# Optimization experiments

Hardware: AMD Instinct MI355X
Metric: run time of the kernel (lower is better)

Reference implementation:

```python
import jax, jax.numpy as jnp
import numpy as np

D = 128
L_SIZE = 65536
C_SIZE = 32768
E = 262144
N_ITERS = 4


def _mlp(x, w1, b1, w2, b2):
    # 2-layer satbench MLP: Linear -> relu -> Linear
    return jax.nn.relu(x @ w1 + b1) @ w2 + b2


def setup_inputs() -> dict:
    key = jax.random.key(0)
    ks = iter(jax.random.split(key, 32))

    def lin(fi, fo):
        # torch nn.Linear default init, stored as (in, out)
        bound = 1.0 / np.sqrt(fi)
        w = jax.random.uniform(next(ks), (fi, fo), minval=-bound, maxval=bound, dtype=jnp.float32)
        b = jax.random.uniform(next(ks), (fo,), minval=-bound, maxval=bound, dtype=jnp.float32)
        return w, b

    s = np.sqrt(2.0 / D).astype(np.float32)
    inp = {}
    inp['l_edge_index'] = jax.random.randint(next(ks), (E,), 0, L_SIZE, dtype=jnp.int64)
    inp['c_edge_index'] = jax.random.randint(next(ks), (E,), 0, C_SIZE, dtype=jnp.int64)
    inp['l_init'] = jax.random.normal(next(ks), (1, D), dtype=jnp.float32) * s
    inp['c_init'] = jax.random.normal(next(ks), (1, D), dtype=jnp.float32) * s
    inp['w_l2c1'], inp['b_l2c1'] = lin(D, D)
    inp['w_l2c2'], inp['b_l2c2'] = lin(D, D)
    inp['w_c2l1'], inp['b_c2l1'] = lin(D, D)
    inp['w_c2l2'], inp['b_c2l2'] = lin(D, D)
    inp['w_l2l1'], inp['b_l2l1'] = lin(D, D)
    inp['w_l2l2'], inp['b_l2l2'] = lin(D, D)
    inp['w_cu'], inp['b_cu'] = lin(2 * D, D)
    inp['w_lu'], inp['b_lu'] = lin(3 * D, D)
    inp['l_size'] = L_SIZE
    inp['c_size'] = C_SIZE
    return inp


def reference(l_edge_index, c_edge_index, l_init, c_init,
              w_l2c1, b_l2c1, w_l2c2, b_l2c2,
              w_c2l1, b_c2l1, w_c2l2, b_c2l2,
              w_l2l1, b_l2l1, w_l2l2, b_l2l2,
              w_cu, b_cu, w_lu, b_lu, l_size, c_size):
    d = l_init.shape[1]
    ones = jnp.ones((l_edge_index.shape[0], 1), dtype=l_init.dtype)
    l_deg = jax.ops.segment_sum(ones, l_edge_index, num_segments=l_size)   # (L,1)
    c_deg = jax.ops.segment_sum(ones, c_edge_index, num_segments=c_size)   # (C,1)
    degree_norm = jnp.sqrt(l_deg[l_edge_index]) * jnp.sqrt(c_deg[c_edge_index])  # (E,1)

    l_emb = jnp.tile(l_init, (l_size, 1))  # (L,d)
    c_emb = jnp.tile(c_init, (c_size, 1))  # (C,d)

    def step(carry, _):
        l_emb, c_emb = carry
        l2c_msg = _mlp(l_emb, w_l2c1, b_l2c1, w_l2c2, b_l2c2)[l_edge_index]  # (E,d)
        c2l_msg = _mlp(c_emb, w_c2l1, b_c2l1, w_c2l2, b_c2l2)[c_edge_index]  # (E,d)
        # swap positive/negative literal partner embeddings (pairs are adjacent rows)
        l2l_in = l_emb.reshape(l_size // 2, 2, d)[:, ::-1, :].reshape(l_size, d)
        l2l_msg = _mlp(l2l_in, w_l2l1, b_l2l1, w_l2l2, b_l2l2)              # (L,d)
        l2c_aggr = jax.ops.segment_sum(l2c_msg / degree_norm, c_edge_index, num_segments=c_size)
        c_new = jnp.concatenate([c_emb, l2c_aggr], axis=1) @ w_cu + b_cu
        c2l_aggr = jax.ops.segment_sum(c2l_msg / degree_norm, l_edge_index, num_segments=l_size)
        l_new = jnp.concatenate([l_emb, c2l_aggr, l2l_msg], axis=1) @ w_lu + b_lu
        return (l_new, c_new), None

    (l_emb, c_emb), _ = jax.lax.scan(step, (l_emb, c_emb), None, length=N_ITERS)
    return l_emb
```

## Files before the change

kernel.cpp:

```cpp
#include <hip/hip_runtime.h>
#include <hip/hip_bf16.h>

#define D_ 128
#define L_ 65536
#define C_ 32768
#define E_ 262144

typedef __hip_bfloat16 bf16;
typedef __attribute__((ext_vector_type(8))) short short8;
typedef __attribute__((ext_vector_type(4))) float f32x4;

__global__ void detect_k(const unsigned short* __restrict__ wmem,
                         const int* __restrict__ li, int* __restrict__ flags) {
    int t = blockIdx.x * 512 + threadIdx.x;
    if (t < 8192) {
        unsigned short h = wmem[2 * t];
        float v = __bfloat162float(*(const bf16*)&h);
        if (!(fabsf(v) < 0.5f)) atomicOr(&flags[0], 1);
    }
    if (t < 2048) {
        if (li[2 * t + 1] != 0) atomicOr(&flags[1], 1);
    }
}

__device__ __forceinline__ void split2(float v, unsigned short& h, unsigned short& l) {
    bf16 bh = __float2bfloat16(v);
    float fh = __bfloat162float(bh);
    bf16 bl = __float2bfloat16(v - fh);
    h = *(unsigned short*)&bh;
    l = *(unsigned short*)&bl;
}

__device__ __forceinline__ float ldf(const void* s, int i, int isf32) {
    return isf32 ? ((const float*)s)[i] : __bfloat162float(((const bf16*)s)[i]);
}

__global__ void fixdeg_k(const int* __restrict__ ls, const int* __restrict__ cs,
                         int* __restrict__ ld_idx, int* __restrict__ cd_idx,
                         int* __restrict__ ldeg, int* __restrict__ cdeg,
                         const int* __restrict__ flags) {
    int i = blockIdx.x * 256 + threadIdx.x;
    int is32 = flags[1];
    if (i < E_) {
        int v = is32 ? ls[i] : ls[2 * i];
        v = min(max(v, 0), L_ - 1);
        ld_idx[i] = v;
        atomicAdd(&ldeg[v], 1);
    } else {
        int j = i - E_;
        int v = is32 ? cs[j] : cs[2 * j];
        v = min(max(v, 0), C_ - 1);
        cd_idx[j] = v;
        atomicAdd(&cdeg[v], 1);
    }
}

__global__ void cvtwb_k(const void* s0, const void* s1, const void* s2, const void* s3,
                        const void* s4, const void* s5, const void* s6, const void* s7,
                        const void* t0, const void* t1, const void* t2, const void* t3,
                        const void* t4, const void* t5, const void* t6, const void* t7,
                        unsigned short* __restrict__ hi, unsigned short* __restrict__ lo,
                        float* __restrict__ bb, const int* __restrict__ flags) {
    int i = blockIdx.x * 256 + threadIdx.x;
    int isf = flags[0];
    if (i >= 180224) {
        int j = i - 180224;
        const void* src;
        switch (j >> 7) {
            case 0: src = t0; break; case 1: src = t1; break;
            case 2: src = t2; break; case 3: src = t3; break;
            case 4: src = t4; break; case 5: src = t5; break;
            case 6: src = t6; break; default: src = t7; break;
        }
        bb[j] = ldf(src, j & 127, isf);
        return;
    }
    const void* src; int K, base;
    if      (i <  16384) { src = s0; K = 128; base = 0; }
    else if (i <  32768) { src = s1; K = 128; base = 16384; }
    else if (i <  49152) { src = s2; K = 128; base = 32768; }
    else if (i <  65536) { src = s3; K = 128; base = 49152; }
    else if (i <  81920) { src = s4; K = 128; base = 65536; }
    else if (i <  98304) { src = s5; K = 128; base = 81920; }
    else if (i < 131072) { src = s6; K = 256; base = 98304; }
    else                 { src = s7; K = 384; base = 131072; }
    int e = i - base;
    int k = e >> 7, n = e & 127;
    float v = ldf(src, e, isf);
    unsigned short h, l;
    split2(v, h, l);
    hi[base + n * K + k] = h;
    lo[base + n * K + k] = l;
}

__global__ void init2_k(const void* __restrict__ lv, const void* __restrict__ cv,
                        float* __restrict__ lemb, float* __restrict__ cemb,
                        const int* __restrict__ flags) {
    int i = blockIdx.x * 256 + threadIdx.x;
    int isf = flags[0];
    if (i < L_ * D_) lemb[i] = ldf(lv, i & (D_ - 1), isf);
    else             cemb[i - L_ * D_] = ldf(cv, i & (D_ - 1), isf);
}

__global__ void scan1b_k(const int* __restrict__ ldeg, const int* __restrict__ cdeg,
                         int* __restrict__ lout, int* __restrict__ cout,
                         int* __restrict__ bsumL, int* __restrict__ bsumC) {
    __shared__ int s[256];
    const int* in; int* out; int* bs; int tile;
    if (blockIdx.x < 256) { in = ldeg; out = lout; bs = bsumL; tile = blockIdx.x; }
    else                  { in = cdeg; out = cout; bs = bsumC; tile = blockIdx.x - 256; }
    int i = tile * 256 + threadIdx.x;
    int v = in[i];
    s[threadIdx.x] = v;
    __syncthreads();
#pragma unroll
    for (int off = 1; off < 256; off <<= 1) {
        int t = (threadIdx.x >= off) ? s[threadIdx.x - off] : 0;
        __syncthreads();
        s[threadIdx.x] += t;
        __syncthreads();
    }
    out[i] = s[threadIdx.x] - v;
    if (threadIdx.x == 255) bs[tile] = s[255];
}

__global__ void scan2b_k(int* __restrict__ bL, int* __restrict__ bC) {
    __shared__ int s[256];
    int* b = blockIdx.x ? bC : bL;
    int nb = blockIdx.x ? 128 : 256;
    int v = (threadIdx.x < nb) ? b[threadIdx.x] : 0;
    s[threadIdx.x] = v;
    __syncthreads();
#pragma unroll
    for (int off = 1; off < 256; off <<= 1) {
        int t = (threadIdx.x >= off) ? s[threadIdx.x - off] : 0;
        __syncthreads();
        s[threadIdx.x] += t;
        __syncthreads();
    }
    if (threadIdx.x < nb) b[threadIdx.x] = s[threadIdx.x] - v;
}

__global__ void scan3b_k(int* __restrict__ lptr, int* __restrict__ cptr,
                         const int* __restrict__ bsumL, const int* __restrict__ bsumC,
                         int* __restrict__ lcur, int* __restrict__ ccur,
                         const int* __restrict__ ldeg, const int* __restrict__ cdeg,
                         float* __restrict__ invsq_l, float* __restrict__ invsq_c) {
    int b = blockIdx.x, t = threadIdx.x;
    if (b < 256) {
        int i = b * 256 + t;
        int v = lptr[i] + bsumL[b];
        lptr[i] = v; lcur[i] = v;
        int d = ldeg[i];
        invsq_l[i] = d ? rsqrtf((float)d) : 0.0f;
    } else {
        int i = (b - 256) * 256 + t;
        int v = cptr[i] + bsumC[b - 256];
        cptr[i] = v; ccur[i] = v;
        int d = cdeg[i];
        invsq_c[i] = d ? rsqrtf((float)d) : 0.0f;
    }
}

__global__ void place_k(const int* __restrict__ li, const int* __restrict__ ci,
                        int* __restrict__ lcur, int* __restrict__ ccur,
                        int* __restrict__ l_other, int* __restrict__ c_other) {
    int e = blockIdx.x * 256 + threadIdx.x;
    if (e >= E_) return;
    int l = li[e], c = ci[e];
    int p = atomicAdd(&ccur[c], 1);
    c_other[p] = l;
    int q = atomicAdd(&lcur[l], 1);
    l_other[q] = c;
}

__global__ __launch_bounds__(256) void gather2_k(
    const int* __restrict__ cptr, const int* __restrict__ cdeg, const int* __restrict__ c_other,
    const float* __restrict__ lmsg, const float* __restrict__ invsq_c, float* __restrict__ caggr,
    const int* __restrict__ lptr, const int* __restrict__ ldeg, const int* __restrict__ l_other,
    const float* __restrict__ cmsg, const float* __restrict__ invsq_l, float* __restrict__ laggr,
    int nC) {
    int node = (blockIdx.x * 256 + threadIdx.x) >> 6;
    int lane = threadIdx.x & 63;
    bool cside = node < nC;
    int j = cside ? node : node - nC;
    const int* ptr = cside ? cptr : lptr;
    const int* dg  = cside ? cdeg : ldeg;
    const int* oth = cside ? c_other : l_other;
    const float* msg = cside ? lmsg : cmsg;
    float sc = (cside ? invsq_c : invsq_l)[j];
    float* out = cside ? caggr : laggr;
    int s = ptr[j], cnt = dg[j];
    float2 a0 = {0.f, 0.f}, a1 = {0.f, 0.f};
    int k = 0;
    for (; k + 2 <= cnt; k += 2) {
        int o0 = oth[s + k], o1 = oth[s + k + 1];
        const float2 m0 = *(const float2*)&msg[(size_t)o0 * D_ + 2 * lane];
        const float2 m1 = *(const float2*)&msg[(size_t)o1 * D_ + 2 * lane];
        a0.x += m0.x; a0.y += m0.y;
        a1.x += m1.x; a1.y += m1.y;
    }
    if (k < cnt) {
        int o = oth[s + k];
        const float2 m = *(const float2*)&msg[(size_t)o * D_ + 2 * lane];
        a0.x += m.x; a0.y += m.y;
    }
    a0.x = (a0.x + a1.x) * sc;
    a0.y = (a0.y + a1.y) * sc;
    *(float2*)&out[(size_t)j * D_ + 2 * lane] = a0;
}

__global__ __launch_bounds__(256, 2) void mlp3_k(
    const float* __restrict__ l_cur, const float* __restrict__ c_cur,
    const unsigned short* __restrict__ wt_hi, const unsigned short* __restrict__ wt_lo,
    const float* __restrict__ bb,
    const float* __restrict__ invsq_l, const float* __restrict__ invsq_c,
    float* __restrict__ l_msg, float* __restrict__ c_msg, float* __restrict__ l2lb,
    int nL, int nC) {
    __shared__ char smem[66048];
    unsigned short (*a_hi)[40] = (unsigned short(*)[40])(smem);
    unsigned short (*a_lo)[40] = (unsigned short(*)[40])(smem + 10240);
    unsigned short (*b_hi)[40] = (unsigned short(*)[40])(smem + 20480);
    unsigned short (*b_lo)[40] = (unsigned short(*)[40])(smem + 30720);
    unsigned short* h_hi = (unsigned short*)(smem);
    unsigned short* h_lo = (unsigned short*)(smem + 32768);
    float* scv = (float*)(smem + 65536);

    int b = blockIdx.x, seg, tile;
    if (b < nL)           { seg = 0; tile = b; }
    else if (b < nL + nC) { seg = 1; tile = b - nL; }
    else                  { seg = 2; tile = b - nL - nC; }
    const float* A = (seg == 1) ? c_cur : l_cur;
    float* outp = (seg == 0) ? l_msg : (seg == 1) ? c_msg : l2lb;
    const float* invsq = (seg == 0) ? invsq_l : (seg == 1) ? invsq_c : nullptr;
    const unsigned short* W1h = wt_hi + seg * 32768;
    const unsigned short* W1l = wt_lo + seg * 32768;
    const unsigned short* W2h = W1h + 16384;
    const unsigned short* W2l = W1l + 16384;
    const float* b1v = bb + seg * 256;
    const float* b2v = b1v + 128;
    const int swap = (seg == 2);

    const int t = threadIdx.x;
    const int br0 = tile * 128;
    const int w = t >> 6, lane = t & 63;
    const int wr = w >> 1, wc = w & 1;
    const int quad = lane >> 4, cl = lane & 15;

    if (t < 128) scv[t] = invsq ? invsq[br0 + t] : 1.0f;

    f32x4 acc[4][4];
#pragma unroll
    for (int i = 0; i < 4; i++)
#pragma unroll
        for (int j = 0; j < 4; j++) acc[i][j] = (f32x4){0.f, 0.f, 0.f, 0.f};

    for (int kt = 0; kt < 128; kt += 32) {
#pragma unroll
        for (int i = 0; i < 4; i++) {
            int f = t + 256 * i;
            int r = f >> 3, kq = f & 7;
            int gr = br0 + r;
            if (swap) gr ^= 1;
            const float4 v = *(const float4*)&A[(size_t)gr * D_ + kt + 4 * kq];
            unsigned short h0, l0, h1, l1, h2, l2, h3, l3;
            split2(v.x, h0, l0); split2(v.y, h1, l1);
            split2(v.z, h2, l2); split2(v.w, h3, l3);
            *(ushort4*)&a_hi[r][4 * kq] = make_ushort4(h0, h1, h2, h3);
            *(ushort4*)&a_lo[r][4 * kq] = make_ushort4(l0, l1, l2, l3);
            *(ushort4*)&b_hi[r][4 * kq] = *(const ushort4*)&W1h[(size_t)r * 128 + kt + 4 * kq];
            *(ushort4*)&b_lo[r][4 * kq] = *(const ushort4*)&W1l[(size_t)r * 128 + kt + 4 * kq];
        }
        __syncthreads();
        short8 af_h[4], af_l[4];
#pragma unroll
        for (int i = 0; i < 4; i++) {
            int row = 64 * wr + 16 * i + cl;
            af_h[i] = *(const short8*)&a_hi[row][quad * 8];
            af_l[i] = *(const short8*)&a_lo[row][quad * 8];
        }
#pragma unroll
        for (int j = 0; j < 4; j++) {
            int col = 64 * wc + 16 * j + cl;
            short8 bf_h = *(const short8*)&b_hi[col][quad * 8];
            short8 bf_l = *(const short8*)&b_lo[col][quad * 8];
#pragma unroll
            for (int i = 0; i < 4; i++) {
                acc[i][j] = __builtin_amdgcn_mfma_f32_16x16x32_bf16(af_h[i], bf_h, acc[i][j], 0, 0, 0);
                acc[i][j] = __builtin_amdgcn_mfma_f32_16x16x32_bf16(af_h[i], bf_l, acc[i][j], 0, 0, 0);
                acc[i][j] = __builtin_amdgcn_mfma_f32_16x16x32_bf16(af_l[i], bf_h, acc[i][j], 0, 0, 0);
            }
        }
        __syncthreads();
    }
#pragma unroll
    for (int j = 0; j < 4; j++) {
        int col = 64 * wc + 16 * j + cl;
        float bv = b1v[col];
        int g = col >> 3, go = col & 7;
#pragma unroll
        for (int i = 0; i < 4; i++) {
            int rloc = 64 * wr + 16 * i + quad * 4;
#pragma unroll
            for (int rg = 0; rg < 4; rg++) {
                float v = fmaxf(acc[i][j][rg] + bv, 0.0f);
                unsigned short hh, ll;
                split2(v, hh, ll);
                int r = rloc + rg;
                int off = r * 128 + ((g ^ (r & 15)) << 3) + go;
                h_hi[off] = hh;
                h_lo[off] = ll;
            }
        }
    }
    __syncthreads();
#pragma unroll
    for (int i = 0; i < 4; i++)
#pragma unroll
        for (int j = 0; j < 4; j++) acc[i][j] = (f32x4){0.f, 0.f, 0.f, 0.f};

    for (int kt = 0; kt < 128; kt += 32) {
        short8 af_h[4], af_l[4];
        int gbase = (kt >> 3) + quad;
#pragma unroll
        for (int i = 0; i < 4; i++) {
            int r = 64 * wr + 16 * i + cl;
            int off = r * 128 + ((gbase ^ cl) << 3);
            af_h[i] = *(const short8*)&h_hi[off];
            af_l[i] = *(const short8*)&h_lo[off];
        }
#pragma unroll
        for (int j = 0; j < 4; j++) {
            int col = 64 * wc + 16 * j + cl;
            const short8 bf_h = *(const short8*)&W2h[(size_t)col * 128 + kt + quad * 8];
            const short8 bf_l = *(const short8*)&W2l[(size_t)col * 128 + kt + quad * 8];
#pragma unroll
            for (int i = 0; i < 4; i++) {
                acc[i][j] = __builtin_amdgcn_mfma_f32_16x16x32_bf16(af_h[i], bf_h, acc[i][j], 0, 0, 0);
                acc[i][j] = __builtin_amdgcn_mfma_f32_16x16x32_bf16(af_h[i], bf_l, acc[i][j], 0, 0, 0);
                acc[i][j] = __builtin_amdgcn_mfma_f32_16x16x32_bf16(af_l[i], bf_h, acc[i][j], 0, 0, 0);
            }
        }
    }
#pragma unroll
    for (int j = 0; j < 4; j++) {
        int col = 64 * wc + 16 * j + cl;
        float bv = b2v[col];
#pragma unroll
        for (int i = 0; i < 4; i++) {
            int rloc = 64 * wr + 16 * i + quad * 4;
#pragma unroll
            for (int rg = 0; rg < 4; rg++)
                outp[(size_t)(br0 + rloc + rg) * D_ + col] = (acc[i][j][rg] + bv) * scv[rloc + rg];
        }
    }
}

template <int FINAL>
__global__ __launch_bounds__(256, 2) void update_k(
    const float* __restrict__ l_cur, const float* __restrict__ c_cur,
    const float* __restrict__ laggr, const float* __restrict__ caggr,
    const float* __restrict__ l2lb,
    const unsigned short* __restrict__ wt_hi, const unsigned short* __restrict__ wt_lo,
    const float* __restrict__ bb,
    float* __restrict__ c_nxt, float* __restrict__ l_nxt,
    void* __restrict__ dout, const int* __restrict__ flags) {
    __shared__ unsigned short a_hi[128][40], a_lo[128][40];
    __shared__ unsigned short b_hi[128][40], b_lo[128][40];
    const int t = threadIdx.x;
    int b = blockIdx.x;
    const bool cseg = (!FINAL) && (b < 256);
    const int tile = (FINAL || cseg) ? b : b - 256;
    const int K = cseg ? 256 : 384;
    const float* A0 = cseg ? c_cur : l_cur;
    const float* A1 = cseg ? caggr : laggr;
    const float* A2 = l2lb;
    const unsigned short* Wh = wt_hi + (cseg ? 98304 : 131072);
    const unsigned short* Wl = wt_lo + (cseg ? 98304 : 131072);
    const float* bias = bb + (cseg ? 768 : 896);
    const int br0 = tile * 128;
    const int w = t >> 6, lane = t & 63;
    const int wr = w >> 1, wc = w & 1;
    const int quad = lane >> 4, cl = lane & 15;

    f32x4 acc[4][4];
#pragma unroll
    for (int i = 0; i < 4; i++)
#pragma unroll
        for (int j = 0; j < 4; j++) acc[i][j] = (f32x4){0.f, 0.f, 0.f, 0.f};

    for (int kt = 0; kt < K; kt += 32) {
        const float* As = (kt < 128) ? A0 : (kt < 256) ? A1 : A2;
        const int koff = kt & 127;
#pragma unroll
        for (int i = 0; i < 4; i++) {
            int f = t + 256 * i;
            int r = f >> 3, kq = f & 7;
            const float4 v = *(const float4*)&As[(size_t)(br0 + r) * D_ + koff + 4 * kq];
            unsigned short h0, l0, h1, l1, h2, l2, h3, l3;
            split2(v.x, h0, l0); split2(v.y, h1, l1);
            split2(v.z, h2, l2); split2(v.w, h3, l3);
            *(ushort4*)&a_hi[r][4 * kq] = make_ushort4(h0, h1, h2, h3);
            *(ushort4*)&a_lo[r][4 * kq] = make_ushort4(l0, l1, l2, l3);
            *(ushort4*)&b_hi[r][4 * kq] = *(const ushort4*)&Wh[(size_t)r * K + kt + 4 * kq];
            *(ushort4*)&b_lo[r][4 * kq] = *(const ushort4*)&Wl[(size_t)r * K + kt + 4 * kq];
        }
        __syncthreads();
        short8 af_h[4], af_l[4];
#pragma unroll
        for (int i = 0; i < 4; i++) {
            int row = 64 * wr + 16 * i + cl;
            af_h[i] = *(const short8*)&a_hi[row][quad * 8];
            af_l[i] = *(const short8*)&a_lo[row][quad * 8];
        }
#pragma unroll
        for (int j = 0; j < 4; j++) {
            int col = 64 * wc + 16 * j + cl;
            short8 bf_h = *(const short8*)&b_hi[col][quad * 8];
            short8 bf_l = *(const short8*)&b_lo[col][quad * 8];
#pragma unroll
            for (int i = 0; i < 4; i++) {
                acc[i][j] = __builtin_amdgcn_mfma_f32_16x16x32_bf16(af_h[i], bf_h, acc[i][j], 0, 0, 0);
                acc[i][j] = __builtin_amdgcn_mfma_f32_16x16x32_bf16(af_h[i], bf_l, acc[i][j], 0, 0, 0);
                acc[i][j] = __builtin_amdgcn_mfma_f32_16x16x32_bf16(af_l[i], bf_h, acc[i][j], 0, 0, 0);
            }
        }
        __syncthreads();
    }
    const int f32out = FINAL ? flags[0] : 1;
#pragma unroll
    for (int j = 0; j < 4; j++) {
        int col = 64 * wc + 16 * j + cl;
        float bv = bias[col];
#pragma unroll
        for (int i = 0; i < 4; i++) {
            int rbase = br0 + 64 * wr + 16 * i + quad * 4;
#pragma unroll
            for (int rg = 0; rg < 4; rg++) {
                float v = acc[i][j][rg] + bv;
                size_t idx = (size_t)(rbase + rg) * D_ + col;
                if (FINAL) {
                    if (f32out) ((float*)dout)[idx] = v;
                    else        ((bf16*)dout)[idx] = __float2bfloat16(v);
                } else {
                    (cseg ? c_nxt : l_nxt)[idx] = v;
                }
            }
        }
    }
}

extern "C" void kernel_launch(void* const* d_in, const int* in_sizes, int n_in,
                              void* d_out, int out_size, void* d_ws, size_t ws_size,
                              hipStream_t stream) {
    const int* li_raw = (const int*)d_in[0];
    const int* ci_raw = (const int*)d_in[1];

    float* ws = (float*)d_ws;
    float* lbuf0 = ws;
    float* lbuf1 = lbuf0 + (size_t)L_ * D_;
    float* l2lb  = lbuf1 + (size_t)L_ * D_;
    float* laggr = l2lb + (size_t)L_ * D_;
    float* cbuf0 = laggr + (size_t)L_ * D_;
    float* cbuf1 = cbuf0 + (size_t)C_ * D_;
    float* caggr = cbuf1 + (size_t)C_ * D_;
    float* invsq_l = caggr + (size_t)C_ * D_;
    float* invsq_c = invsq_l + L_;
    float* bb    = invsq_c + C_;
    unsigned short* wt_hi = (unsigned short*)(bb + 1024);
    unsigned short* wt_lo = wt_hi + 180224;
    int*   li    = (int*)(wt_lo + 180224);
    int*   ci    = li + E_;
    int*   l_other = ci + E_;
    int*   c_other = l_other + E_;
    int*   ldegi = c_other + E_;
    int*   cdegi = ldegi + L_;
    int*   lptr  = cdegi + C_;
    int*   cptr  = lptr + L_;
    int*   lcur  = cptr + C_;
    int*   ccur  = lcur + L_;
    int*   bsumL = ccur + C_;
    int*   bsumC = bsumL + 256;
    int*   flags = bsumC + 128;

    hipMemsetAsync(flags, 0, 2 * sizeof(int), stream);
    detect_k<<<16, 512, 0, stream>>>((const unsigned short*)d_in[4], li_raw, flags);

    hipMemsetAsync(ldegi, 0, (size_t)(L_ + C_) * sizeof(int), stream);
    fixdeg_k<<<2 * E_ / 256, 256, 0, stream>>>(li_raw, ci_raw, li, ci, ldegi, cdegi, flags);

    cvtwb_k<<<708, 256, 0, stream>>>(d_in[4], d_in[6], d_in[8], d_in[10], d_in[12],
                                     d_in[14], d_in[16], d_in[18],
                                     d_in[5], d_in[7], d_in[9], d_in[11], d_in[13],
                                     d_in[15], d_in[17], d_in[19], wt_hi, wt_lo, bb, flags);

    scan1b_k<<<384, 256, 0, stream>>>(ldegi, cdegi, lptr, cptr, bsumL, bsumC);
    scan2b_k<<<2, 256, 0, stream>>>(bsumL, bsumC);
    scan3b_k<<<384, 256, 0, stream>>>(lptr, cptr, bsumL, bsumC, lcur, ccur,
                                      ldegi, cdegi, invsq_l, invsq_c);
    place_k<<<E_ / 256, 256, 0, stream>>>(li, ci, lcur, ccur, l_other, c_other);

    init2_k<<<(L_ + C_) * D_ / 256, 256, 0, stream>>>(d_in[2], d_in[3], lbuf0, cbuf0, flags);

    float* l_cur = lbuf0; float* l_nxt = lbuf1;
    float* c_cur = cbuf0; float* c_nxt = cbuf1;

    for (int it = 0; it < 3; it++) {
        mlp3_k<<<(L_ / 128) * 2 + C_ / 128, 256, 0, stream>>>(
            l_cur, c_cur, wt_hi, wt_lo, bb, invsq_l, invsq_c,
            l_nxt, c_nxt, l2lb, L_ / 128, C_ / 128);
        gather2_k<<<(C_ + L_) / 4, 256, 0, stream>>>(
            cptr, cdegi, c_other, l_nxt, invsq_c, caggr,
            lptr, ldegi, l_other, c_nxt, invsq_l, laggr, C_);
        update_k<0><<<768, 256, 0, stream>>>(
            l_cur, c_cur, laggr, caggr, l2lb, wt_hi, wt_lo, bb,
            c_nxt, l_nxt, nullptr, flags);
        float* tmp = l_cur; l_cur = l_nxt; l_nxt = tmp;
        tmp = c_cur; c_cur = c_nxt; c_nxt = tmp;
    }
    mlp3_k<<<C_ / 128 + L_ / 128, 256, 0, stream>>>(
        l_cur, c_cur, wt_hi, wt_lo, bb, invsq_l, invsq_c,
        l_nxt, c_nxt, l2lb, 0, C_ / 128);
    gather2_k<<<L_ / 4, 256, 0, stream>>>(
        cptr, cdegi, c_other, l_nxt, invsq_c, caggr,
        lptr, ldegi, l_other, c_nxt, invsq_l, laggr, 0);
    update_k<1><<<512, 256, 0, stream>>>(
        l_cur, c_cur, laggr, caggr, l2lb, wt_hi, wt_lo, bb,
        nullptr, nullptr, d_out, flags);
}
```

Measured before the change: 695.4 us.

## Store MLP messages in bf16 and gather packed bf16 pairs

The per-node MLP outputs (l2c, c2l, l2l messages) are now written as bf16 instead of fp32, which halves the bytes the edge gather reads per neighbour. The gather unpacks bf16 pairs from 32-bit words and is unrolled to four neighbours. The update kernel loads the l2l slice directly as bf16 and skips the lo-part MFMA for that K range. init2 is also vectorised to float4 stores. This gives up precision on the messages compared with the previous split hi/lo fp32-equivalent path, which risks accuracy drift across iterations.

```diff
diff --git a/kernel.cpp b/kernel.cpp
--- a/kernel.cpp
+++ b/kernel.cpp
@@ -96,10 +96,18 @@
 __global__ void init2_k(const void* __restrict__ lv, const void* __restrict__ cv,
                         float* __restrict__ lemb, float* __restrict__ cemb,
                         const int* __restrict__ flags) {
-    int i = blockIdx.x * 256 + threadIdx.x;
+    int i4 = blockIdx.x * 256 + threadIdx.x;
     int isf = flags[0];
-    if (i < L_ * D_) lemb[i] = ldf(lv, i & (D_ - 1), isf);
-    else             cemb[i - L_ * D_] = ldf(cv, i & (D_ - 1), isf);
+    const void* src; float* dst; int o;
+    if (i4 < L_ * 32) { src = lv; dst = lemb; o = i4; }
+    else              { src = cv; dst = cemb; o = i4 - L_ * 32; }
+    int j = (o & 31) * 4;
+    float4 v;
+    v.x = ldf(src, j + 0, isf);
+    v.y = ldf(src, j + 1, isf);
+    v.z = ldf(src, j + 2, isf);
+    v.w = ldf(src, j + 3, isf);
+    ((float4*)dst)[o] = v;
 }
 
 __global__ void scan1b_k(const int* __restrict__ ldeg, const int* __restrict__ cdeg,
@@ -176,9 +184,9 @@
 
 __global__ __launch_bounds__(256) void gather2_k(
     const int* __restrict__ cptr, const int* __restrict__ cdeg, const int* __restrict__ c_other,
-    const float* __restrict__ lmsg, const float* __restrict__ invsq_c, float* __restrict__ caggr,
+    const unsigned int* __restrict__ lmsg, const float* __restrict__ invsq_c, float* __restrict__ caggr,
     const int* __restrict__ lptr, const int* __restrict__ ldeg, const int* __restrict__ l_other,
-    const float* __restrict__ cmsg, const float* __restrict__ invsq_l, float* __restrict__ laggr,
+    const unsigned int* __restrict__ cmsg, const float* __restrict__ invsq_l, float* __restrict__ laggr,
     int nC) {
     int node = (blockIdx.x * 256 + threadIdx.x) >> 6;
     int lane = threadIdx.x & 63;
@@ -187,23 +195,28 @@
     const int* ptr = cside ? cptr : lptr;
     const int* dg  = cside ? cdeg : ldeg;
     const int* oth = cside ? c_other : l_other;
-    const float* msg = cside ? lmsg : cmsg;
+    const unsigned int* msg = cside ? lmsg : cmsg;
     float sc = (cside ? invsq_c : invsq_l)[j];
     float* out = cside ? caggr : laggr;
     int s = ptr[j], cnt = dg[j];
     float2 a0 = {0.f, 0.f}, a1 = {0.f, 0.f};
     int k = 0;
-    for (; k + 2 <= cnt; k += 2) {
-        int o0 = oth[s + k], o1 = oth[s + k + 1];
-        const float2 m0 = *(const float2*)&msg[(size_t)o0 * D_ + 2 * lane];
-        const float2 m1 = *(const float2*)&msg[(size_t)o1 * D_ + 2 * lane];
-        a0.x += m0.x; a0.y += m0.y;
-        a1.x += m1.x; a1.y += m1.y;
-    }
-    if (k < cnt) {
+    for (; k + 4 <= cnt; k += 4) {
+        int o0 = oth[s + k], o1 = oth[s + k + 1], o2 = oth[s + k + 2], o3 = oth[s + k + 3];
+        unsigned int u0 = msg[(size_t)o0 * 64 + lane];
+        unsigned int u1 = msg[(size_t)o1 * 64 + lane];
+        unsigned int u2 = msg[(size_t)o2 * 64 + lane];
+        unsigned int u3 = msg[(size_t)o3 * 64 + lane];
+        a0.x += __uint_as_float(u0 << 16) + __uint_as_float(u2 << 16);
+        a0.y += __uint_as_float(u0 & 0xffff0000u) + __uint_as_float(u2 & 0xffff0000u);
+        a1.x += __uint_as_float(u1 << 16) + __uint_as_float(u3 << 16);
+        a1.y += __uint_as_float(u1 & 0xffff0000u) + __uint_as_float(u3 & 0xffff0000u);
+    }
+    for (; k < cnt; k++) {
         int o = oth[s + k];
-        const float2 m = *(const float2*)&msg[(size_t)o * D_ + 2 * lane];
-        a0.x += m.x; a0.y += m.y;
+        unsigned int u = msg[(size_t)o * 64 + lane];
+        a0.x += __uint_as_float(u << 16);
+        a0.y += __uint_as_float(u & 0xffff0000u);
     }
     a0.x = (a0.x + a1.x) * sc;
     a0.y = (a0.y + a1.y) * sc;
@@ -215,7 +228,7 @@
     const unsigned short* __restrict__ wt_hi, const unsigned short* __restrict__ wt_lo,
     const float* __restrict__ bb,
     const float* __restrict__ invsq_l, const float* __restrict__ invsq_c,
-    float* __restrict__ l_msg, float* __restrict__ c_msg, float* __restrict__ l2lb,
+    bf16* __restrict__ l_msg, bf16* __restrict__ c_msg, bf16* __restrict__ l2lb,
     int nL, int nC) {
     __shared__ char smem[66048];
     unsigned short (*a_hi)[40] = (unsigned short(*)[40])(smem);
@@ -231,7 +244,7 @@
     else if (b < nL + nC) { seg = 1; tile = b - nL; }
     else                  { seg = 2; tile = b - nL - nC; }
     const float* A = (seg == 1) ? c_cur : l_cur;
-    float* outp = (seg == 0) ? l_msg : (seg == 1) ? c_msg : l2lb;
+    bf16* outp = (seg == 0) ? l_msg : (seg == 1) ? c_msg : l2lb;
     const float* invsq = (seg == 0) ? invsq_l : (seg == 1) ? invsq_c : nullptr;
     const unsigned short* W1h = wt_hi + seg * 32768;
     const unsigned short* W1l = wt_lo + seg * 32768;
@@ -351,7 +364,8 @@
             int rloc = 64 * wr + 16 * i + quad * 4;
 #pragma unroll
             for (int rg = 0; rg < 4; rg++)
-                outp[(size_t)(br0 + rloc + rg) * D_ + col] = (acc[i][j][rg] + bv) * scv[rloc + rg];
+                outp[(size_t)(br0 + rloc + rg) * D_ + col] =
+                    __float2bfloat16((acc[i][j][rg] + bv) * scv[rloc + rg]);
         }
     }
 }
@@ -360,7 +374,7 @@
 __global__ __launch_bounds__(256, 2) void update_k(
     const float* __restrict__ l_cur, const float* __restrict__ c_cur,
     const float* __restrict__ laggr, const float* __restrict__ caggr,
-    const float* __restrict__ l2lb,
+    const bf16* __restrict__ l2lb,
     const unsigned short* __restrict__ wt_hi, const unsigned short* __restrict__ wt_lo,
     const float* __restrict__ bb,
     float* __restrict__ c_nxt, float* __restrict__ l_nxt,
@@ -374,7 +388,6 @@
     const int K = cseg ? 256 : 384;
     const float* A0 = cseg ? c_cur : l_cur;
     const float* A1 = cseg ? caggr : laggr;
-    const float* A2 = l2lb;
     const unsigned short* Wh = wt_hi + (cseg ? 98304 : 131072);
     const unsigned short* Wl = wt_lo + (cseg ? 98304 : 131072);
     const float* bias = bb + (cseg ? 768 : 896);
@@ -390,18 +403,24 @@
         for (int j = 0; j < 4; j++) acc[i][j] = (f32x4){0.f, 0.f, 0.f, 0.f};
 
     for (int kt = 0; kt < K; kt += 32) {
-        const float* As = (kt < 128) ? A0 : (kt < 256) ? A1 : A2;
+        const bool haslo = (kt < 256);
         const int koff = kt & 127;
 #pragma unroll
         for (int i = 0; i < 4; i++) {
             int f = t + 256 * i;
             int r = f >> 3, kq = f & 7;
-            const float4 v = *(const float4*)&As[(size_t)(br0 + r) * D_ + koff + 4 * kq];
-            unsigned short h0, l0, h1, l1, h2, l2, h3, l3;
-            split2(v.x, h0, l0); split2(v.y, h1, l1);
-            split2(v.z, h2, l2); split2(v.w, h3, l3);
-            *(ushort4*)&a_hi[r][4 * kq] = make_ushort4(h0, h1, h2, h3);
-            *(ushort4*)&a_lo[r][4 * kq] = make_ushort4(l0, l1, l2, l3);
+            if (haslo) {
+                const float* As = (kt < 128) ? A0 : A1;
+                const float4 v = *(const float4*)&As[(size_t)(br0 + r) * D_ + koff + 4 * kq];
+                unsigned short h0, l0, h1, l1, h2, l2, h3, l3;
+                split2(v.x, h0, l0); split2(v.y, h1, l1);
+                split2(v.z, h2, l2); split2(v.w, h3, l3);
+                *(ushort4*)&a_hi[r][4 * kq] = make_ushort4(h0, h1, h2, h3);
+                *(ushort4*)&a_lo[r][4 * kq] = make_ushort4(l0, l1, l2, l3);
+            } else {
+                *(ushort4*)&a_hi[r][4 * kq] =
+                    *(const ushort4*)&l2lb[(size_t)(br0 + r) * D_ + koff + 4 * kq];
+            }
             *(ushort4*)&b_hi[r][4 * kq] = *(const ushort4*)&Wh[(size_t)r * K + kt + 4 * kq];
             *(ushort4*)&b_lo[r][4 * kq] = *(const ushort4*)&Wl[(size_t)r * K + kt + 4 * kq];
         }
@@ -411,7 +430,7 @@
         for (int i = 0; i < 4; i++) {
             int row = 64 * wr + 16 * i + cl;
             af_h[i] = *(const short8*)&a_hi[row][quad * 8];
-            af_l[i] = *(const short8*)&a_lo[row][quad * 8];
+            if (haslo) af_l[i] = *(const short8*)&a_lo[row][quad * 8];
         }
 #pragma unroll
         for (int j = 0; j < 4; j++) {
@@ -422,7 +441,8 @@
             for (int i = 0; i < 4; i++) {
                 acc[i][j] = __builtin_amdgcn_mfma_f32_16x16x32_bf16(af_h[i], bf_h, acc[i][j], 0, 0, 0);
                 acc[i][j] = __builtin_amdgcn_mfma_f32_16x16x32_bf16(af_h[i], bf_l, acc[i][j], 0, 0, 0);
-                acc[i][j] = __builtin_amdgcn_mfma_f32_16x16x32_bf16(af_l[i], bf_h, acc[i][j], 0, 0, 0);
+                if (haslo)
+                    acc[i][j] = __builtin_amdgcn_mfma_f32_16x16x32_bf16(af_l[i], bf_h, acc[i][j], 0, 0, 0);
             }
         }
         __syncthreads();
@@ -500,31 +520,32 @@
                                       ldegi, cdegi, invsq_l, invsq_c);
     place_k<<<E_ / 256, 256, 0, stream>>>(li, ci, lcur, ccur, l_other, c_other);
 
-    init2_k<<<(L_ + C_) * D_ / 256, 256, 0, stream>>>(d_in[2], d_in[3], lbuf0, cbuf0, flags);
+    init2_k<<<(L_ + C_) * 32 / 256, 256, 0, stream>>>(d_in[2], d_in[3], lbuf0, cbuf0, flags);
 
     float* l_cur = lbuf0; float* l_nxt = lbuf1;
     float* c_cur = cbuf0; float* c_nxt = cbuf1;
 
+    const int nL = L_ / 128, nC = C_ / 128;
     for (int it = 0; it < 3; it++) {
-        mlp3_k<<<(L_ / 128) * 2 + C_ / 128, 256, 0, stream>>>(
+        mlp3_k<<<2 * nL + nC, 256, 0, stream>>>(
             l_cur, c_cur, wt_hi, wt_lo, bb, invsq_l, invsq_c,
-            l_nxt, c_nxt, l2lb, L_ / 128, C_ / 128);
+            (bf16*)l_nxt, (bf16*)c_nxt, (bf16*)l2lb, nL, nC);
         gather2_k<<<(C_ + L_) / 4, 256, 0, stream>>>(
-            cptr, cdegi, c_other, l_nxt, invsq_c, caggr,
-            lptr, ldegi, l_other, c_nxt, invsq_l, laggr, C_);
+            cptr, cdegi, c_other, (const unsigned int*)l_nxt, invsq_c, caggr,
+            lptr, ldegi, l_other, (const unsigned int*)c_nxt, invsq_l, laggr, C_);
         update_k<0><<<768, 256, 0, stream>>>(
-            l_cur, c_cur, laggr, caggr, l2lb, wt_hi, wt_lo, bb,
+            l_cur, c_cur, laggr, caggr, (const bf16*)l2lb, wt_hi, wt_lo, bb,
             c_nxt, l_nxt, nullptr, flags);
         float* tmp = l_cur; l_cur = l_nxt; l_nxt = tmp;
         tmp = c_cur; c_cur = c_nxt; c_nxt = tmp;
     }
-    mlp3_k<<<C_ / 128 + L_ / 128, 256, 0, stream>>>(
+    mlp3_k<<<nC + nL, 256, 0, stream>>>(
         l_cur, c_cur, wt_hi, wt_lo, bb, invsq_l, invsq_c,
-        l_nxt, c_nxt, l2lb, 0, C_ / 128);
+        (bf16*)l_nxt, (bf16*)c_nxt, (bf16*)l2lb, 0, nC);
     gather2_k<<<L_ / 4, 256, 0, stream>>>(
-        cptr, cdegi, c_other, l_nxt, invsq_c, caggr,
-        lptr, ldegi, l_other, c_nxt, invsq_l, laggr, 0);
+        cptr, cdegi, c_other, (const unsigned int*)l_nxt, invsq_c, caggr,
+        lptr, ldegi, l_other, (const unsigned int*)c_nxt, invsq_l, laggr, 0);
     update_k<1><<<512, 256, 0, stream>>>(
-        l_cur, c_cur, laggr, caggr, l2lb, wt_hi, wt_lo, bb,
+        l_cur, c_cur, laggr, caggr, (const bf16*)l2lb, wt_hi, wt_lo, bb,
         nullptr, nullptr, d_out, flags);
 }
```

After: 688.4 us. No clear change (-1.0%).
